# Performance work log

Measured on AMD Instinct MI355X. Metric: run time of the kernel, lower is better.

## Reference

```python
import jax, jax.numpy as jnp
import numpy as np

DIM = 512
HEADS = 8
HEAD_DIM = DIM // HEADS
SCALE = HEAD_DIM ** -0.5
CPB_HIDDEN = 512
N_CLASSES = 2
LN_EPS = 1e-5


def _layernorm(x, g, b):
    m = jnp.mean(x, axis=-1, keepdims=True)
    v = jnp.var(x, axis=-1, keepdims=True)
    return (x - m) / jnp.sqrt(v + LN_EPS) * g + b


def _coord_attention(x, coords, cpb_w1, cpb_b1, cpb_w2, cpb_b2, qkv_w, qkv_b, proj_w, proj_b):
    B, N, C = x.shape
    qkv = (x @ qkv_w + qkv_b).reshape(B, N, 3, HEADS, HEAD_DIM)
    q, k, v = jnp.moveaxis(qkv, 2, 0)  # each (B, N, H, hd)
    attn = jnp.einsum('bnhd,bmhd->bhnm', q * SCALE, k)  # (B, H, N, N)
    rel = coords[:, :, None, :] - coords[:, None, :, :]  # (B, N, N, 2)
    rel = rel / (jnp.linalg.norm(rel, axis=-1, keepdims=True) + 1e-6)
    bias = jax.nn.relu(rel @ cpb_w1 + cpb_b1) @ cpb_w2 + cpb_b2  # (B, N, N, H)
    attn = jax.nn.softmax(attn + jnp.transpose(bias, (0, 3, 1, 2)), axis=-1)
    out = jnp.einsum('bhnm,bmhd->bnhd', attn, v).reshape(B, N, C)
    return out @ proj_w + proj_b


def setup_inputs() -> dict:
    key = jax.random.key(0)
    ks = iter(jax.random.split(key, 32))
    d = {}
    d['h'] = jax.random.normal(next(ks), (1, 400, 1024), dtype=jnp.float32)
    d['coords'] = jax.random.uniform(next(ks), (1, 400, 2), dtype=jnp.float32) * 1000.0
    def lin(kw, kb, fan_in, fan_out):
        w = jax.random.normal(kw, (fan_in, fan_out), dtype=jnp.float32) / np.sqrt(fan_in)
        b = jax.random.normal(kb, (fan_out,), dtype=jnp.float32) * 0.01
        return w, b
    d['fc1_w'], d['fc1_b'] = lin(next(ks), next(ks), 1024, DIM)
    d['cls_token'] = jax.random.normal(next(ks), (1, 1, DIM), dtype=jnp.float32)
    for p in ('l1', 'l2'):
        d[p + '_norm_g'] = jnp.ones((DIM,), jnp.float32)
        d[p + '_norm_b'] = jnp.zeros((DIM,), jnp.float32)
        d[p + '_cpb_w1'], d[p + '_cpb_b1'] = lin(next(ks), next(ks), 2, CPB_HIDDEN)
        d[p + '_cpb_w2'], d[p + '_cpb_b2'] = lin(next(ks), next(ks), CPB_HIDDEN, HEADS)
        d[p + '_qkv_w'], d[p + '_qkv_b'] = lin(next(ks), next(ks), DIM, 3 * DIM)
        d[p + '_proj_w'], d[p + '_proj_b'] = lin(next(ks), next(ks), DIM, DIM)
    d['norm_g'] = jnp.ones((DIM,), jnp.float32)
    d['norm_b'] = jnp.zeros((DIM,), jnp.float32)
    d['fc2_w'], d['fc2_b'] = lin(next(ks), next(ks), DIM, N_CLASSES)
    return d


def reference(h, coords, fc1_w, fc1_b, cls_token,
              l1_norm_g, l1_norm_b, l1_cpb_w1, l1_cpb_b1, l1_cpb_w2, l1_cpb_b2,
              l1_qkv_w, l1_qkv_b, l1_proj_w, l1_proj_b,
              l2_norm_g, l2_norm_b, l2_cpb_w1, l2_cpb_b1, l2_cpb_w2, l2_cpb_b2,
              l2_qkv_w, l2_qkv_b, l2_proj_w, l2_proj_b,
              norm_g, norm_b, fc2_w, fc2_b):
    B, Np, _ = h.shape
    h = jax.nn.relu(h @ fc1_w + fc1_b)  # (B, N, 512)
    side = int(np.ceil(np.sqrt(Np)))
    add = side * side - Np  # pad bag to a perfect square (wrap-around copy)
    h = jnp.concatenate([h, h[:, :add, :]], axis=1)
    coords = jnp.concatenate([coords, coords[:, :add, :]], axis=1)
    cls = jnp.broadcast_to(cls_token, (B, 1, DIM))
    h = jnp.concatenate([cls, h], axis=1)
    coords = jnp.concatenate([jnp.zeros((B, 1, 2), h.dtype), coords], axis=1)
    h = h + _coord_attention(_layernorm(h, l1_norm_g, l1_norm_b), coords,
                             l1_cpb_w1, l1_cpb_b1, l1_cpb_w2, l1_cpb_b2,
                             l1_qkv_w, l1_qkv_b, l1_proj_w, l1_proj_b)
    h = h + _coord_attention(_layernorm(h, l2_norm_g, l2_norm_b), coords,
                             l2_cpb_w1, l2_cpb_b1, l2_cpb_w2, l2_cpb_b2,
                             l2_qkv_w, l2_qkv_b, l2_proj_w, l2_proj_b)
    h = _layernorm(h, norm_g, norm_b)[:, 0]  # CLS token
    return h @ fc2_w + fc2_b  # (B, n_classes)
```

## Files before the change

### kernel.cpp

```cpp
#include <hip/hip_runtime.h>
#include <math.h>

#define NP 401
#define DIM 512
#define LN_EPS 1e-5f
#define ATT_SCALE 0.125f
#define CPB_M 4096
#define TSTRIDE (CPB_M + 64)
#define PQS (401L * 1536)
#define PKS (401L * 1024)
#define PVS (401L * 512)

template<bool TB, typename LA, typename LB>
__device__ __forceinline__ void gemm64(
    int kBeg, int kEnd, int tid,
    float (*as)[68], float (*bs)[68], float (&acc)[4][4],
    LA&& loadA, LB&& loadB)
{
    float aR[4], bR[4];
    loadA(kBeg, aR);
    loadB(kBeg, bR);
    for (int k0 = kBeg; k0 < kEnd; k0 += 16) {
        const int arow = tid >> 2, aq = tid & 3;
        as[aq * 4 + 0][arow] = aR[0];
        as[aq * 4 + 1][arow] = aR[1];
        as[aq * 4 + 2][arow] = aR[2];
        as[aq * 4 + 3][arow] = aR[3];
        if (!TB) {
            *(float4*)&bs[tid >> 4][(tid & 15) * 4] =
                make_float4(bR[0], bR[1], bR[2], bR[3]);
        } else {
            bs[aq * 4 + 0][arow] = bR[0];
            bs[aq * 4 + 1][arow] = bR[1];
            bs[aq * 4 + 2][arow] = bR[2];
            bs[aq * 4 + 3][arow] = bR[3];
        }
        __syncthreads();
        float nA[4] = {0.f,0.f,0.f,0.f}, nB[4] = {0.f,0.f,0.f,0.f};
        if (k0 + 16 < kEnd) { loadA(k0 + 16, nA); loadB(k0 + 16, nB); }
        const int tx = tid & 15, ty = tid >> 4;
        #pragma unroll
        for (int kk = 0; kk < 16; ++kk) {
            float4 a4 = *(const float4*)&as[kk][ty * 4];
            float4 b4 = *(const float4*)&bs[kk][tx * 4];
            float av[4] = {a4.x, a4.y, a4.z, a4.w};
            float bv[4] = {b4.x, b4.y, b4.z, b4.w};
            #pragma unroll
            for (int r = 0; r < 4; ++r)
                #pragma unroll
                for (int c = 0; c < 4; ++c)
                    acc[r][c] = fmaf(av[r], bv[c], acc[r][c]);
        }
        __syncthreads();
        #pragma unroll
        for (int j = 0; j < 4; ++j) { aR[j] = nA[j]; bR[j] = nB[j]; }
    }
}

__global__ __launch_bounds__(256) void gemm_split_kernel(
    const float* __restrict__ A, int lda,
    const float* __restrict__ B, int ldb,
    float* __restrict__ P, int ldc, long slice,
    int M, int N, int K, int skN)
{
    __shared__ float as[16][68], bs[16][68];
    const int tid = threadIdx.x;
    const int m0 = blockIdx.x * 64, n0 = blockIdx.y * 64;
    const int sk = blockIdx.z;
    const int KS = ((K + skN * 16 - 1) / (skN * 16)) * 16;
    const int kBeg = sk * KS;
    const int kEnd = (kBeg + KS < K) ? kBeg + KS : K;
    float acc[4][4] = {};

    auto loadA = [&](int k0, float r[4]) {
        r[0] = r[1] = r[2] = r[3] = 0.f;
        int gm = m0 + (tid >> 2);
        if (gm >= M) return;
        int gk = k0 + (tid & 3) * 4;
        const float* p = A + (long)gm * lda + gk;
        if (gk + 3 < kEnd) {
            float4 v = *(const float4*)p;
            r[0] = v.x; r[1] = v.y; r[2] = v.z; r[3] = v.w;
        } else {
            #pragma unroll
            for (int j = 0; j < 4; ++j) if (gk + j < kEnd) r[j] = p[j];
        }
    };
    auto loadB = [&](int k0, float r[4]) {
        r[0] = r[1] = r[2] = r[3] = 0.f;
        int gk = k0 + (tid >> 4);
        if (gk >= kEnd) return;
        int gn = n0 + (tid & 15) * 4;
        const float* p = B + (long)gk * ldb + gn;
        float4 v = *(const float4*)p;
        r[0] = v.x; r[1] = v.y; r[2] = v.z; r[3] = v.w;
    };
    if (kBeg < kEnd)
        gemm64<false>(kBeg, kEnd, tid, as, bs, acc, loadA, loadB);

    float* C = P + (long)sk * slice;
    const int tx = tid & 15, ty = tid >> 4;
    #pragma unroll
    for (int r = 0; r < 4; ++r) {
        int m = m0 + ty * 4 + r;
        if (m >= M) continue;
        *(float4*)&C[(long)m * ldc + n0 + tx * 4] =
            make_float4(acc[r][0], acc[r][1], acc[r][2], acc[r][3]);
    }
}

__global__ __launch_bounds__(256) void reduce_kernel(
    const float* __restrict__ P, long slice, int skN,
    const float* __restrict__ bias, float* __restrict__ out,
    int total, int N)
{
    int idx = (blockIdx.x * 256 + threadIdx.x) * 4;
    if (idx >= total) return;
    float4 s = *(const float4*)(P + idx);
    for (int k = 1; k < skN; ++k) {
        float4 p = *(const float4*)(P + (long)k * slice + idx);
        s.x += p.x; s.y += p.y; s.z += p.z; s.w += p.w;
    }
    if (bias) {
        const float4 b = *(const float4*)(bias + (idx % N));
        s.x += b.x; s.y += b.y; s.z += b.z; s.w += b.w;
    }
    *(float4*)(out + idx) = s;
}

__global__ __launch_bounds__(256) void flash_kernel(
    const float* __restrict__ qkv,
    const int* __restrict__ pm, const float* __restrict__ pf,
    const float* __restrict__ T,
    float* __restrict__ PO,
    float* __restrict__ Pml)
{
    __shared__ float as[16][68], bs[16][68];
    __shared__ float pT[64][68];
    __shared__ float vs[64][68];
    const int tid = threadIdx.x;
    const int m0 = blockIdx.x * 64, nb = blockIdx.y, h = blockIdx.z;
    const int n0 = nb * 64;
    float acc[4][4] = {};

    float vreg[4][4];
    {
        int key = n0 + (tid >> 2);
        int d0 = (tid & 3) * 16;
        if (key <= 400) {
            const float* p = qkv + (long)key * 1536 + 1024 + h * 64 + d0;
            #pragma unroll
            for (int i = 0; i < 4; ++i) {
                float4 v = *(const float4*)(p + i * 4);
                vreg[i][0] = v.x; vreg[i][1] = v.y;
                vreg[i][2] = v.z; vreg[i][3] = v.w;
            }
        } else {
            #pragma unroll
            for (int i = 0; i < 4; ++i)
                vreg[i][0] = vreg[i][1] = vreg[i][2] = vreg[i][3] = 0.f;
        }
    }

    auto loadQ = [&](int k0, float r[4]) {
        int gm = m0 + (tid >> 2);
        if (gm > 400) { r[0]=r[1]=r[2]=r[3]=0.f; return; }
        int gk = k0 + (tid & 3) * 4;
        float4 v = *(const float4*)(qkv + (long)gm * 1536 + h * 64 + gk);
        r[0]=v.x; r[1]=v.y; r[2]=v.z; r[3]=v.w;
    };
    auto loadK = [&](int k0, float r[4]) {
        int gn = n0 + (tid >> 2);
        if (gn > 400) { r[0]=r[1]=r[2]=r[3]=0.f; return; }
        int gk = k0 + (tid & 3) * 4;
        float4 v = *(const float4*)(qkv + (long)gn * 1536 + 512 + h * 64 + gk);
        r[0]=v.x; r[1]=v.y; r[2]=v.z; r[3]=v.w;
    };
    gemm64<true>(0, 64, tid, as, bs, acc, loadQ, loadK);

    {
        int key = tid >> 2, d0 = (tid & 3) * 16;
        #pragma unroll
        for (int i = 0; i < 4; ++i)
            *(float4*)&vs[key][d0 + i * 4] =
                make_float4(vreg[i][0], vreg[i][1], vreg[i][2], vreg[i][3]);
    }

    const int tx = tid & 15, ty = tid >> 4;
    const float* Tt = T + (long)h * TSTRIDE;
    float p[4][4];
    #pragma unroll
    for (int r = 0; r < 4; ++r) {
        int i = m0 + ty * 4 + r;
        float sv[4];
        #pragma unroll
        for (int c = 0; c < 4; ++c) {
            int j = n0 + tx * 4 + c;
            if (i <= 400 && j <= 400) {
                int id = i * 416 + j;
                int mm = pm[id];
                float fr = pf[id];
                float t0 = Tt[mm], t1 = Tt[mm + 1];
                sv[c] = fmaf(acc[r][c], ATT_SCALE, fmaf(fr, t1 - t0, t0));
            } else {
                sv[c] = -INFINITY;
            }
        }
        float cmax = fmaxf(fmaxf(sv[0], sv[1]), fmaxf(sv[2], sv[3]));
        cmax = fmaxf(cmax, __shfl_xor(cmax, 1));
        cmax = fmaxf(cmax, __shfl_xor(cmax, 2));
        cmax = fmaxf(cmax, __shfl_xor(cmax, 4));
        cmax = fmaxf(cmax, __shfl_xor(cmax, 8));
        const bool rowok = (i <= 400);
        #pragma unroll
        for (int c = 0; c < 4; ++c)
            p[r][c] = rowok ? __expf(sv[c] - cmax) : 0.f;
        float cs = p[r][0] + p[r][1] + p[r][2] + p[r][3];
        cs += __shfl_xor(cs, 1);
        cs += __shfl_xor(cs, 2);
        cs += __shfl_xor(cs, 4);
        cs += __shfl_xor(cs, 8);
        if (tx == 0 && rowok) {
            long o = ((long)(h * 401 + i) * 7 + nb) * 2;
            Pml[o] = cmax;
            Pml[o + 1] = cs;
        }
    }
    #pragma unroll
    for (int c = 0; c < 4; ++c)
        *(float4*)&pT[tx * 4 + c][ty * 4] =
            make_float4(p[0][c], p[1][c], p[2][c], p[3][c]);
    __syncthreads();

    float o[4][4] = {};
    #pragma unroll 16
    for (int kk = 0; kk < 64; ++kk) {
        float4 a4 = *(const float4*)&pT[kk][ty * 4];
        float4 b4 = *(const float4*)&vs[kk][tx * 4];
        float av[4] = {a4.x, a4.y, a4.z, a4.w};
        float bv[4] = {b4.x, b4.y, b4.z, b4.w};
        #pragma unroll
        for (int r = 0; r < 4; ++r)
            #pragma unroll
            for (int c = 0; c < 4; ++c)
                o[r][c] = fmaf(av[r], bv[c], o[r][c]);
    }

    float* C = PO + (long)nb * PVS;
    #pragma unroll
    for (int r = 0; r < 4; ++r) {
        int m = m0 + ty * 4 + r;
        if (m > 400) continue;
        *(float4*)&C[(long)m * 512 + h * 64 + tx * 4] =
            make_float4(o[r][0], o[r][1], o[r][2], o[r][3]);
    }
}

__global__ __launch_bounds__(256) void proj_kernel(
    const float* __restrict__ PO, const float* __restrict__ Pml,
    const float* __restrict__ projw, float* __restrict__ Pp)
{
    __shared__ float as[16][68], bs[16][68];
    __shared__ float wls[64][8];
    const int tid = threadIdx.x;
    const int m0 = blockIdx.x * 64, n0 = blockIdx.y * 64, sk = blockIdx.z;
    const int kBeg = sk * 64, kEnd = kBeg + 64;
    float acc[4][4] = {};

    if (tid < 64) {
        int row = m0 + tid;
        if (row <= 400) {
            const float* q = Pml + ((long)(sk * 401 + row) * 7) * 2;
            float M = -INFINITY;
            #pragma unroll
            for (int c = 0; c < 7; ++c) M = fmaxf(M, q[c * 2]);
            float D = 0.f;
            #pragma unroll
            for (int c = 0; c < 7; ++c) D += q[c * 2 + 1] * __expf(q[c * 2] - M);
            float iD = 1.f / D;
            #pragma unroll
            for (int c = 0; c < 7; ++c) wls[tid][c] = __expf(q[c * 2] - M) * iD;
        } else {
            #pragma unroll
            for (int c = 0; c < 7; ++c) wls[tid][c] = 0.f;
        }
    }
    __syncthreads();

    auto loadA = [&](int k0, float r4[4]) {
        r4[0] = r4[1] = r4[2] = r4[3] = 0.f;
        int lm = tid >> 2, gm = m0 + lm;
        if (gm > 400) return;
        int gk = k0 + (tid & 3) * 4;
        #pragma unroll
        for (int s = 0; s < 7; ++s) {
            float4 v = *(const float4*)(PO + (long)s * PVS + (long)gm * 512 + gk);
            float w = wls[lm][s];
            r4[0] = fmaf(w, v.x, r4[0]);
            r4[1] = fmaf(w, v.y, r4[1]);
            r4[2] = fmaf(w, v.z, r4[2]);
            r4[3] = fmaf(w, v.w, r4[3]);
        }
    };
    auto loadB = [&](int k0, float r[4]) {
        int gk = k0 + (tid >> 4);
        int gn = n0 + (tid & 15) * 4;
        float4 v = *(const float4*)(projw + (long)gk * 512 + gn);
        r[0]=v.x; r[1]=v.y; r[2]=v.z; r[3]=v.w;
    };
    gemm64<false>(kBeg, kEnd, tid, as, bs, acc, loadA, loadB);

    float* C = Pp + (long)sk * PVS;
    const int tx = tid & 15, ty = tid >> 4;
    #pragma unroll
    for (int r = 0; r < 4; ++r) {
        int m = m0 + ty * 4 + r;
        if (m > 400) continue;
        *(float4*)&C[(long)m * 512 + n0 + tx * 4] =
            make_float4(acc[r][0], acc[r][1], acc[r][2], acc[r][3]);
    }
}

__global__ __launch_bounds__(256) void rowfuse_kernel(
    const float* __restrict__ P, long slice, int skN, int rowOff,
    const float* __restrict__ bias, int doRelu,
    const float* __restrict__ resid, const float* __restrict__ cls,
    float* __restrict__ h0,
    const float* __restrict__ g, const float* __restrict__ b,
    float* __restrict__ xln)
{
    const int r = blockIdx.x, t = threadIdx.x;
    float v0, v1;
    if (cls && r == 0) {
        v0 = cls[t]; v1 = cls[t + 256];
    } else {
        const float* p = P + (long)(r - rowOff) * DIM;
        v0 = bias[t]; v1 = bias[t + 256];
        for (int k = 0; k < skN; ++k) {
            v0 += p[(long)k * slice + t];
            v1 += p[(long)k * slice + t + 256];
        }
        if (resid) {
            v0 += resid[(long)r * DIM + t];
            v1 += resid[(long)r * DIM + t + 256];
        }
        if (doRelu) { v0 = fmaxf(v0, 0.f); v1 = fmaxf(v1, 0.f); }
    }
    h0[(long)r * DIM + t] = v0;
    h0[(long)r * DIM + t + 256] = v1;

    float s = v0 + v1, sq = v0 * v0 + v1 * v1;
    #pragma unroll
    for (int off = 32; off > 0; off >>= 1) {
        s += __shfl_down(s, off);
        sq += __shfl_down(sq, off);
    }
    __shared__ float ps[4], pq[4];
    int w = t >> 6, lane = t & 63;
    if (lane == 0) { ps[w] = s; pq[w] = sq; }
    __syncthreads();
    float Sm = ps[0] + ps[1] + ps[2] + ps[3];
    float Q = pq[0] + pq[1] + pq[2] + pq[3];
    float mean = Sm * (1.f / DIM);
    float var = Q * (1.f / DIM) - mean * mean;
    float inv = rsqrtf(var + LN_EPS);
    xln[(long)r * DIM + t]       = (v0 - mean) * inv * g[t] + b[t];
    xln[(long)r * DIM + t + 256] = (v1 - mean) * inv * g[t + 256] + b[t + 256];
}

__global__ __launch_bounds__(256) void cls_decode_kernel(
    const float* __restrict__ xln, const float* __restrict__ qkvw,
    const float* __restrict__ Pkv, const float* __restrict__ qkvb,
    const int* __restrict__ pm, const float* __restrict__ pf,
    const float* __restrict__ T,
    float* __restrict__ cms, float* __restrict__ cpv,
    unsigned* __restrict__ cnt)
{
    const int h = blockIdx.x, c = blockIdx.y, tid = threadIdx.x;
    const int kBeg = c * 64;
    __shared__ float q0[64], scraw[64], p[64], red[4][64], rr[2];

    if (h == 0 && c == 0 && tid == 0) *cnt = 0u;

    {
        int d = tid & 63, w4 = tid >> 6;
        const float* col = qkvw + h * 64 + d;
        float acc = 0.f;
        for (int k = w4 * 128; k < w4 * 128 + 128; ++k)
            acc = fmaf(xln[k], col[(long)k * 1536], acc);
        red[w4][d] = acc;
    }
    __syncthreads();
    if (tid < 64)
        q0[tid] = red[0][tid] + red[1][tid] + red[2][tid] + red[3][tid]
                  + qkvb[h * 64 + tid];
    __syncthreads();

    {
        int k = tid >> 2, q = tid & 3;
        int j = kBeg + k;
        float dot = 0.f;
        if (j < NP) {
            long base = (long)j * 1024 + h * 64 + q * 16;
            #pragma unroll
            for (int d = 0; d < 16; d += 4) {
                float4 x0 = *(const float4*)(Pkv + base + d);
                float4 x1 = *(const float4*)(Pkv + PKS + base + d);
                float4 x2 = *(const float4*)(Pkv + 2 * PKS + base + d);
                float4 x3 = *(const float4*)(Pkv + 3 * PKS + base + d);
                float4 bb = *(const float4*)(qkvb + 512 + h * 64 + q * 16 + d);
                float4 qq = *(const float4*)(q0 + q * 16 + d);
                dot = fmaf(qq.x, x0.x + x1.x + x2.x + x3.x + bb.x, dot);
                dot = fmaf(qq.y, x0.y + x1.y + x2.y + x3.y + bb.y, dot);
                dot = fmaf(qq.z, x0.z + x1.z + x2.z + x3.z + bb.z, dot);
                dot = fmaf(qq.w, x0.w + x1.w + x2.w + x3.w + bb.w, dot);
            }
        }
        dot += __shfl_down(dot, 2);
        dot += __shfl_down(dot, 1);
        if (q == 0) scraw[k] = dot;
    }
    __syncthreads();

    if (tid < 64) {
        int j = kBeg + tid;
        float s;
        if (j < NP) {
            int mm = pm[j];
            float fr = pf[j];
            const float* Tt = T + (long)h * TSTRIDE;
            float t0 = Tt[mm], t1 = Tt[mm + 1];
            s = fmaf(scraw[tid], ATT_SCALE, fmaf(fr, t1 - t0, t0));
        } else {
            s = -INFINITY;
        }
        float m = s;
        #pragma unroll
        for (int off = 32; off > 0; off >>= 1)
            m = fmaxf(m, __shfl_xor(m, off));
        float e = (j < NP) ? __expf(s - m) : 0.f;
        float sum = e;
        #pragma unroll
        for (int off = 32; off > 0; off >>= 1)
            sum += __shfl_xor(sum, off);
        p[tid] = e;
        if (tid == 0) { rr[0] = m; rr[1] = sum; }
    }
    __syncthreads();

    {
        int w = tid >> 6, d = tid & 63;
        float vb = qkvb[1024 + h * 64 + d];
        float acc = 0.f;
        for (int k = w; k < 64; k += 4) {
            int j = kBeg + k;
            if (j >= NP) break;
            long o = (long)j * 1024 + 512 + h * 64 + d;
            float v = Pkv[o] + Pkv[PKS + o] + Pkv[2 * PKS + o]
                      + Pkv[3 * PKS + o] + vb;
            acc = fmaf(p[k], v, acc);
        }
        red[w][d] = acc;
    }
    __syncthreads();
    if (tid < 64) {
        cpv[((long)h * 7 + c) * 64 + tid] =
            red[0][tid] + red[1][tid] + red[2][tid] + red[3][tid];
        if (tid == 0) {
            cms[(h * 7 + c) * 2 + 0] = rr[0];
            cms[(h * 7 + c) * 2 + 1] = rr[1];
        }
    }
}

__global__ __launch_bounds__(256) void cls_proj_kernel(
    const float* __restrict__ cms, const float* __restrict__ cpv,
    const float* __restrict__ projw, const float* __restrict__ projb,
    float* __restrict__ proj0,
    const float* __restrict__ h0,
    const float* __restrict__ g, const float* __restrict__ b,
    const float* __restrict__ fc2w, const float* __restrict__ fc2b,
    float* __restrict__ out, unsigned* __restrict__ cnt)
{
    __shared__ float av[512], red[4][64];
    __shared__ int isLast;
    const int bk = blockIdx.x, tid = threadIdx.x;
    for (int d = tid; d < 512; d += 256) {
        int h = d >> 6, dd = d & 63;
        float M = -INFINITY;
        #pragma unroll
        for (int c = 0; c < 7; ++c)
            M = fmaxf(M, cms[(h * 7 + c) * 2]);
        float Sx = 0.f, acc = 0.f;
        #pragma unroll
        for (int c = 0; c < 7; ++c) {
            float e = __expf(cms[(h * 7 + c) * 2] - M);
            Sx += cms[(h * 7 + c) * 2 + 1] * e;
            acc += cpv[((long)h * 7 + c) * 64 + dd] * e;
        }
        av[d] = acc / Sx;
    }
    __syncthreads();
    int gg = tid >> 6, n = bk * 64 + (tid & 63);
    float acc = 0.f;
    for (int k = gg * 128; k < gg * 128 + 128; ++k)
        acc = fmaf(av[k], projw[(long)k * 512 + n], acc);
    red[gg][tid & 63] = acc;
    __syncthreads();
    if (tid < 64)
        proj0[bk * 64 + tid] = red[0][tid] + red[1][tid] + red[2][tid]
                               + red[3][tid] + projb[bk * 64 + tid];

    __threadfence();
    if (tid == 0) isLast = (atomicAdd(cnt, 1u) == 7u);
    __syncthreads();
    if (!isLast) return;
    __threadfence();

    const int t = tid;
    float v0 = h0[t] + proj0[t];
    float v1 = h0[t + 256] + proj0[t + 256];
    float s = v0 + v1, sq = v0 * v0 + v1 * v1;
    #pragma unroll
    for (int off = 32; off > 0; off >>= 1) {
        s += __shfl_down(s, off);
        sq += __shfl_down(sq, off);
    }
    __shared__ float ps[4], pq[4], pc0[4], pc1[4];
    int w = t >> 6, lane = t & 63;
    if (lane == 0) { ps[w] = s; pq[w] = sq; }
    __syncthreads();
    float Sm = ps[0] + ps[1] + ps[2] + ps[3];
    float Q = pq[0] + pq[1] + pq[2] + pq[3];
    float mean = Sm * (1.f / DIM);
    float var = Q * (1.f / DIM) - mean * mean;
    float inv = rsqrtf(var + LN_EPS);
    float n0 = (v0 - mean) * inv * g[t] + b[t];
    float n1 = (v1 - mean) * inv * g[t + 256] + b[t + 256];
    float c0 = n0 * fc2w[t * 2]     + n1 * fc2w[(t + 256) * 2];
    float c1 = n0 * fc2w[t * 2 + 1] + n1 * fc2w[(t + 256) * 2 + 1];
    #pragma unroll
    for (int off = 32; off > 0; off >>= 1) {
        c0 += __shfl_down(c0, off);
        c1 += __shfl_down(c1, off);
    }
    if (lane == 0) { pc0[w] = c0; pc1[w] = c1; }
    __syncthreads();
    if (t == 0) {
        out[0] = pc0[0] + pc0[1] + pc0[2] + pc0[3] + fc2b[0];
        out[1] = pc1[0] + pc1[1] + pc1[2] + pc1[3] + fc2b[1];
    }
}

__global__ __launch_bounds__(256) void mega_kernel(
    const float* __restrict__ hin, const float* __restrict__ fc1_w,
    const float* __restrict__ w1_0, const float* __restrict__ b1_0,
    const float* __restrict__ w2_0, const float* __restrict__ b2_0,
    const float* __restrict__ w1_1, const float* __restrict__ b1_1,
    const float* __restrict__ w2_1, const float* __restrict__ b2_1,
    const float* __restrict__ coords,
    float* __restrict__ Pp, float* __restrict__ T,
    int* __restrict__ pm, float* __restrict__ pf)
{
    __shared__ float smem[2176];
    float (*as)[68] = (float(*)[68])smem;
    float (*bs)[68] = (float(*)[68])(smem + 1088);
    float (*red)[64][8] = (float(*)[64][8])smem;
    const int bid = blockIdx.x, tid = threadIdx.x;

    if (bid < 896) {
        int sk = bid / 56, rem = bid % 56;
        int m0 = (rem % 7) * 64, n0 = (rem / 7) * 64;
        int kBeg = sk * 64, kEnd = kBeg + 64;
        float acc[4][4] = {};
        auto loadA = [&](int k0, float r[4]) {
            r[0]=r[1]=r[2]=r[3]=0.f;
            int gm = m0 + (tid >> 2);
            if (gm >= 400) return;
            int gk = k0 + (tid & 3) * 4;
            float4 v = *(const float4*)(hin + (long)gm * 1024 + gk);
            r[0]=v.x; r[1]=v.y; r[2]=v.z; r[3]=v.w;
        };
        auto loadB = [&](int k0, float r[4]) {
            int gk = k0 + (tid >> 4);
            int gn = n0 + (tid & 15) * 4;
            float4 v = *(const float4*)(fc1_w + (long)gk * 512 + gn);
            r[0]=v.x; r[1]=v.y; r[2]=v.z; r[3]=v.w;
        };
        gemm64<false>(kBeg, kEnd, tid, as, bs, acc, loadA, loadB);
        float* C = Pp + (long)sk * PVS;
        const int tx = tid & 15, ty = tid >> 4;
        #pragma unroll
        for (int r = 0; r < 4; ++r) {
            int m = m0 + ty * 4 + r;
            if (m >= 400) continue;
            *(float4*)&C[(long)m * 512 + n0 + tx * 4] =
                make_float4(acc[r][0], acc[r][1], acc[r][2], acc[r][3]);
        }
    } else if (bid < 1026) {
        int tb = bid - 896;
        int z = tb / 65, ab = tb % 65;
        const float* w1 = z ? w1_1 : w1_0;
        const float* b1 = z ? b1_1 : b1_0;
        const float* w2 = z ? w2_1 : w2_0;
        const float* b2 = z ? b2_1 : b2_0;
        const int lane = tid & 63, wv = tid >> 6;
        float ca = 0.f, sa = 0.f;
        if (ab != 64) {
            float th = fmaf((float)(ab * 64 + lane),
                            (float)(2.0 * M_PI / CPB_M), -(float)M_PI);
            sincosf(th, &sa, &ca);
        } else if (lane == 0) {
            sincosf((float)M_PI, &sa, &ca);
        }
        float a8[8] = {};
        const int kbeg = wv * 128;
        #pragma unroll 4
        for (int k = kbeg; k < kbeg + 128; ++k) {
            float hk = fmaxf(fmaf(ca, w1[k],
                                  fmaf(sa, w1[512 + k], b1[k])), 0.f);
            #pragma unroll
            for (int h2 = 0; h2 < 8; ++h2)
                a8[h2] = fmaf(hk, w2[k * 8 + h2], a8[h2]);
        }
        #pragma unroll
        for (int h2 = 0; h2 < 8; ++h2) red[wv][lane][h2] = a8[h2];
        __syncthreads();
        if (tid < 64) {
            int aidx = ab * 64 + tid;
            if (aidx <= CPB_M + 1) {
                #pragma unroll
                for (int h2 = 0; h2 < 8; ++h2)
                    T[(long)(z * 8 + h2) * TSTRIDE + aidx] =
                        red[0][tid][h2] + red[1][tid][h2] +
                        red[2][tid][h2] + red[3][tid][h2] + b2[h2];
            }
        }
    } else {
        int p = (bid - 1026) * 256 + tid;
        if (p < NP * NP) {
            int i = p / NP, j = p - i * NP;
            float xi = (i == 0) ? 0.f : coords[(i - 1) * 2];
            float yi = (i == 0) ? 0.f : coords[(i - 1) * 2 + 1];
            float xj = (j == 0) ? 0.f : coords[(j - 1) * 2];
            float yj = (j == 0) ? 0.f : coords[(j - 1) * 2 + 1];
            float rx = xi - xj, ry = yi - yj;
            int mm; float fr;
            if (rx == 0.f && ry == 0.f) {
                mm = CPB_M + 1; fr = 0.f;
            } else {
                float x = (atan2f(ry, rx) + 3.14159265358979f)
                          * (float)(CPB_M / (2.0 * M_PI));
                int mi = (int)x;
                fr = x - (float)mi;
                mm = (mi >= CPB_M) ? mi - CPB_M : mi;
            }
            pm[i * 416 + j] = mm;
            pf[i * 416 + j] = fr;
        }
    }
}

extern "C" void kernel_launch(void* const* d_in, const int* in_sizes, int n_in,
                              void* d_out, int out_size, void* d_ws, size_t ws_size,
                              hipStream_t stream)
{
    const float* coords = (const float*)d_in[1];
    float* ws = (float*)d_ws;
    float* h0   = ws;                    ws += 401L * 512;
    float* xln  = ws;                    ws += 401L * 512;
    float* PO   = ws;                    ws += 7L * PVS;
    float* T    = ws;                    ws += 16L * TSTRIDE;
    int*   pm   = (int*)ws;              ws += 401L * 416;
    float* pf   = ws;                    ws += 401L * 416;
    float* Pq   = ws;                    ws += 4L * PQS;
    float* qkv  = ws;                    ws += 401L * 1536;
    float* Pp   = ws;                    ws += 16L * PVS;
    float* proj0 = ws;                   ws += 512;
    float* cms  = ws;                    ws += 8L * 7 * 2;
    float* cpv  = ws;                    ws += 8L * 7 * 64;
    float* Pml  = ws;                    ws += 8L * 401 * 7 * 2;
    unsigned* cnt = (unsigned*)ws;       ws += 16;

    mega_kernel<<<1655, 256, 0, stream>>>(
        (const float*)d_in[0], (const float*)d_in[2],
        (const float*)d_in[7],  (const float*)d_in[8],
        (const float*)d_in[9],  (const float*)d_in[10],
        (const float*)d_in[17], (const float*)d_in[18],
        (const float*)d_in[19], (const float*)d_in[20],
        coords, Pp, T, pm, pf);

    rowfuse_kernel<<<401, 256, 0, stream>>>(
        Pp, PVS, 16, 1, (const float*)d_in[3], 1, nullptr,
        (const float*)d_in[4], h0,
        (const float*)d_in[5], (const float*)d_in[6], xln);

    gemm_split_kernel<<<dim3(7, 24, 4), 256, 0, stream>>>(
        xln, 512, (const float*)d_in[11], 1536, Pq, 1536, PQS,
        401, 1536, 512, 4);
    reduce_kernel<<<602, 256, 0, stream>>>(
        Pq, PQS, 4, (const float*)d_in[12], qkv, 401 * 1536, 1536);
    flash_kernel<<<dim3(7, 7, 8), 256, 0, stream>>>(
        qkv, pm, pf, T, PO, Pml);
    proj_kernel<<<dim3(7, 8, 8), 256, 0, stream>>>(
        PO, Pml, (const float*)d_in[13], Pp);
    rowfuse_kernel<<<401, 256, 0, stream>>>(
        Pp, PVS, 8, 0, (const float*)d_in[14], 0, h0, nullptr, h0,
        (const float*)d_in[15], (const float*)d_in[16], xln);

    gemm_split_kernel<<<dim3(7, 16, 4), 256, 0, stream>>>(
        xln, 512, (const float*)d_in[21] + 512, 1536, Pq, 1024, PKS,
        401, 1024, 512, 4);
    cls_decode_kernel<<<dim3(8, 7), 256, 0, stream>>>(
        xln, (const float*)d_in[21], Pq, (const float*)d_in[22],
        pm, pf, T + 8L * TSTRIDE, cms, cpv, cnt);
    cls_proj_kernel<<<8, 256, 0, stream>>>(
        cms, cpv, (const float*)d_in[23], (const float*)d_in[24], proj0,
        h0, (const float*)d_in[25], (const float*)d_in[26],
        (const float*)d_in[27], (const float*)d_in[28], (float*)d_out, cnt);
}
```

Measured before the change: 241.3 us.

## Drop split-K partial sums for QKV/KV GEMMs and fuse bias into epilogue

Replaces the split-K GEMM plus separate reduce kernel with a single full-K GEMM that adds the bias directly, so one launch and the partial-sum round trip through global memory go away. The layer-2 KV projection now writes final values, which simplifies cls_decode loads. The fc1 split-K inside mega_kernel drops from 16 to 4 slices, shrinking partial buffers and rowfuse reduction work. The cost is fewer blocks (168/112 instead of 4x that), which lowers parallelism on a large GPU and leaves each block with a longer serial K loop.

```diff
diff --git a/kernel.cpp b/kernel.cpp
--- a/kernel.cpp
+++ b/kernel.cpp
@@ -7,8 +7,6 @@
 #define ATT_SCALE 0.125f
 #define CPB_M 4096
 #define TSTRIDE (CPB_M + 64)
-#define PQS (401L * 1536)
-#define PKS (401L * 1024)
 #define PVS (401L * 512)
 
 template<bool TB, typename LA, typename LB>
@@ -57,75 +55,42 @@
     }
 }
 
-__global__ __launch_bounds__(256) void gemm_split_kernel(
-    const float* __restrict__ A, int lda,
+__global__ __launch_bounds__(256) void gemm_bias_kernel(
+    const float* __restrict__ A,
     const float* __restrict__ B, int ldb,
-    float* __restrict__ P, int ldc, long slice,
-    int M, int N, int K, int skN)
+    const float* __restrict__ bias,
+    float* __restrict__ C, int ldc)
 {
     __shared__ float as[16][68], bs[16][68];
     const int tid = threadIdx.x;
     const int m0 = blockIdx.x * 64, n0 = blockIdx.y * 64;
-    const int sk = blockIdx.z;
-    const int KS = ((K + skN * 16 - 1) / (skN * 16)) * 16;
-    const int kBeg = sk * KS;
-    const int kEnd = (kBeg + KS < K) ? kBeg + KS : K;
     float acc[4][4] = {};
 
     auto loadA = [&](int k0, float r[4]) {
-        r[0] = r[1] = r[2] = r[3] = 0.f;
         int gm = m0 + (tid >> 2);
-        if (gm >= M) return;
+        if (gm > 400) { r[0]=r[1]=r[2]=r[3]=0.f; return; }
         int gk = k0 + (tid & 3) * 4;
-        const float* p = A + (long)gm * lda + gk;
-        if (gk + 3 < kEnd) {
-            float4 v = *(const float4*)p;
-            r[0] = v.x; r[1] = v.y; r[2] = v.z; r[3] = v.w;
-        } else {
-            #pragma unroll
-            for (int j = 0; j < 4; ++j) if (gk + j < kEnd) r[j] = p[j];
-        }
+        float4 v = *(const float4*)(A + (long)gm * 512 + gk);
+        r[0]=v.x; r[1]=v.y; r[2]=v.z; r[3]=v.w;
     };
     auto loadB = [&](int k0, float r[4]) {
-        r[0] = r[1] = r[2] = r[3] = 0.f;
         int gk = k0 + (tid >> 4);
-        if (gk >= kEnd) return;
         int gn = n0 + (tid & 15) * 4;
-        const float* p = B + (long)gk * ldb + gn;
-        float4 v = *(const float4*)p;
-        r[0] = v.x; r[1] = v.y; r[2] = v.z; r[3] = v.w;
+        float4 v = *(const float4*)(B + (long)gk * ldb + gn);
+        r[0]=v.x; r[1]=v.y; r[2]=v.z; r[3]=v.w;
     };
-    if (kBeg < kEnd)
-        gemm64<false>(kBeg, kEnd, tid, as, bs, acc, loadA, loadB);
-
-    float* C = P + (long)sk * slice;
+    gemm64<false>(0, 512, tid, as, bs, acc, loadA, loadB);
+
     const int tx = tid & 15, ty = tid >> 4;
+    const float4 bv = *(const float4*)(bias + n0 + tx * 4);
     #pragma unroll
     for (int r = 0; r < 4; ++r) {
         int m = m0 + ty * 4 + r;
-        if (m >= M) continue;
+        if (m > 400) continue;
         *(float4*)&C[(long)m * ldc + n0 + tx * 4] =
-            make_float4(acc[r][0], acc[r][1], acc[r][2], acc[r][3]);
-    }
-}
-
-__global__ __launch_bounds__(256) void reduce_kernel(
-    const float* __restrict__ P, long slice, int skN,
-    const float* __restrict__ bias, float* __restrict__ out,
-    int total, int N)
-{
-    int idx = (blockIdx.x * 256 + threadIdx.x) * 4;
-    if (idx >= total) return;
-    float4 s = *(const float4*)(P + idx);
-    for (int k = 1; k < skN; ++k) {
-        float4 p = *(const float4*)(P + (long)k * slice + idx);
-        s.x += p.x; s.y += p.y; s.z += p.z; s.w += p.w;
-    }
-    if (bias) {
-        const float4 b = *(const float4*)(bias + (idx % N));
-        s.x += b.x; s.y += b.y; s.z += b.z; s.w += b.w;
-    }
-    *(float4*)(out + idx) = s;
+            make_float4(acc[r][0] + bv.x, acc[r][1] + bv.y,
+                        acc[r][2] + bv.z, acc[r][3] + bv.w);
+    }
 }
 
 __global__ __launch_bounds__(256) void flash_kernel(
@@ -370,7 +335,7 @@
 
 __global__ __launch_bounds__(256) void cls_decode_kernel(
     const float* __restrict__ xln, const float* __restrict__ qkvw,
-    const float* __restrict__ Pkv, const float* __restrict__ qkvb,
+    const float* __restrict__ kv, const float* __restrict__ qkvb,
     const int* __restrict__ pm, const float* __restrict__ pf,
     const float* __restrict__ T,
     float* __restrict__ cms, float* __restrict__ cpv,
@@ -404,16 +369,12 @@
             long base = (long)j * 1024 + h * 64 + q * 16;
             #pragma unroll
             for (int d = 0; d < 16; d += 4) {
-                float4 x0 = *(const float4*)(Pkv + base + d);
-                float4 x1 = *(const float4*)(Pkv + PKS + base + d);
-                float4 x2 = *(const float4*)(Pkv + 2 * PKS + base + d);
-                float4 x3 = *(const float4*)(Pkv + 3 * PKS + base + d);
-                float4 bb = *(const float4*)(qkvb + 512 + h * 64 + q * 16 + d);
+                float4 x0 = *(const float4*)(kv + base + d);
                 float4 qq = *(const float4*)(q0 + q * 16 + d);
-                dot = fmaf(qq.x, x0.x + x1.x + x2.x + x3.x + bb.x, dot);
-                dot = fmaf(qq.y, x0.y + x1.y + x2.y + x3.y + bb.y, dot);
-                dot = fmaf(qq.z, x0.z + x1.z + x2.z + x3.z + bb.z, dot);
-                dot = fmaf(qq.w, x0.w + x1.w + x2.w + x3.w + bb.w, dot);
+                dot = fmaf(qq.x, x0.x, dot);
+                dot = fmaf(qq.y, x0.y, dot);
+                dot = fmaf(qq.z, x0.z, dot);
+                dot = fmaf(qq.w, x0.w, dot);
             }
         }
         dot += __shfl_down(dot, 2);
@@ -450,15 +411,12 @@
 
     {
         int w = tid >> 6, d = tid & 63;
-        float vb = qkvb[1024 + h * 64 + d];
         float acc = 0.f;
         for (int k = w; k < 64; k += 4) {
             int j = kBeg + k;
             if (j >= NP) break;
             long o = (long)j * 1024 + 512 + h * 64 + d;
-            float v = Pkv[o] + Pkv[PKS + o] + Pkv[2 * PKS + o]
-                      + Pkv[3 * PKS + o] + vb;
-            acc = fmaf(p[k], v, acc);
+            acc = fmaf(p[k], kv[o], acc);
         }
         red[w][d] = acc;
     }
@@ -568,10 +526,10 @@
     float (*red)[64][8] = (float(*)[64][8])smem;
     const int bid = blockIdx.x, tid = threadIdx.x;
 
-    if (bid < 896) {
+    if (bid < 224) {
         int sk = bid / 56, rem = bid % 56;
         int m0 = (rem % 7) * 64, n0 = (rem / 7) * 64;
-        int kBeg = sk * 64, kEnd = kBeg + 64;
+        int kBeg = sk * 256, kEnd = kBeg + 256;
         float acc[4][4] = {};
         auto loadA = [&](int k0, float r[4]) {
             r[0]=r[1]=r[2]=r[3]=0.f;
@@ -597,8 +555,8 @@
             *(float4*)&C[(long)m * 512 + n0 + tx * 4] =
                 make_float4(acc[r][0], acc[r][1], acc[r][2], acc[r][3]);
         }
-    } else if (bid < 1026) {
-        int tb = bid - 896;
+    } else if (bid < 354) {
+        int tb = bid - 224;
         int z = tb / 65, ab = tb % 65;
         const float* w1 = z ? w1_1 : w1_0;
         const float* b1 = z ? b1_1 : b1_0;
@@ -637,7 +595,7 @@
             }
         }
     } else {
-        int p = (bid - 1026) * 256 + tid;
+        int p = (bid - 354) * 256 + tid;
         if (p < NP * NP) {
             int i = p / NP, j = p - i * NP;
             float xi = (i == 0) ? 0.f : coords[(i - 1) * 2];
@@ -673,16 +631,16 @@
     float* T    = ws;                    ws += 16L * TSTRIDE;
     int*   pm   = (int*)ws;              ws += 401L * 416;
     float* pf   = ws;                    ws += 401L * 416;
-    float* Pq   = ws;                    ws += 4L * PQS;
+    float* kv   = ws;                    ws += 401L * 1024;
     float* qkv  = ws;                    ws += 401L * 1536;
-    float* Pp   = ws;                    ws += 16L * PVS;
+    float* Pp   = ws;                    ws += 8L * PVS;
     float* proj0 = ws;                   ws += 512;
     float* cms  = ws;                    ws += 8L * 7 * 2;
     float* cpv  = ws;                    ws += 8L * 7 * 64;
     float* Pml  = ws;                    ws += 8L * 401 * 7 * 2;
     unsigned* cnt = (unsigned*)ws;       ws += 16;
 
-    mega_kernel<<<1655, 256, 0, stream>>>(
+    mega_kernel<<<983, 256, 0, stream>>>(
         (const float*)d_in[0], (const float*)d_in[2],
         (const float*)d_in[7],  (const float*)d_in[8],
         (const float*)d_in[9],  (const float*)d_in[10],
@@ -691,15 +649,13 @@
         coords, Pp, T, pm, pf);
 
     rowfuse_kernel<<<401, 256, 0, stream>>>(
-        Pp, PVS, 16, 1, (const float*)d_in[3], 1, nullptr,
+        Pp, PVS, 4, 1, (const float*)d_in[3], 1, nullptr,
         (const float*)d_in[4], h0,
         (const float*)d_in[5], (const float*)d_in[6], xln);
 
-    gemm_split_kernel<<<dim3(7, 24, 4), 256, 0, stream>>>(
-        xln, 512, (const float*)d_in[11], 1536, Pq, 1536, PQS,
-        401, 1536, 512, 4);
-    reduce_kernel<<<602, 256, 0, stream>>>(
-        Pq, PQS, 4, (const float*)d_in[12], qkv, 401 * 1536, 1536);
+    gemm_bias_kernel<<<dim3(7, 24), 256, 0, stream>>>(
+        xln, (const float*)d_in[11], 1536, (const float*)d_in[12],
+        qkv, 1536);
     flash_kernel<<<dim3(7, 7, 8), 256, 0, stream>>>(
         qkv, pm, pf, T, PO, Pml);
     proj_kernel<<<dim3(7, 8, 8), 256, 0, stream>>>(
@@ -708,11 +664,11 @@
         Pp, PVS, 8, 0, (const float*)d_in[14], 0, h0, nullptr, h0,
         (const float*)d_in[15], (const float*)d_in[16], xln);
 
-    gemm_split_kernel<<<dim3(7, 16, 4), 256, 0, stream>>>(
-        xln, 512, (const float*)d_in[21] + 512, 1536, Pq, 1024, PKS,
-        401, 1024, 512, 4);
+    gemm_bias_kernel<<<dim3(7, 16), 256, 0, stream>>>(
+        xln, (const float*)d_in[21] + 512, 1536, (const float*)d_in[22] + 512,
+        kv, 1024);
     cls_decode_kernel<<<dim3(8, 7), 256, 0, stream>>>(
-        xln, (const float*)d_in[21], Pq, (const float*)d_in[22],
+        xln, (const float*)d_in[21], kv, (const float*)d_in[22],
         pm, pf, T + 8L * TSTRIDE, cms, cpv, cnt);
     cls_proj_kernel<<<8, 256, 0, stream>>>(
         cms, cpv, (const float*)d_in[23], (const float*)d_in[24], proj0,
```

New measurement: 242.7 us. No clear change (+0.6%).

## Fuse QKV split-K reduction into flash kernel loads and halve fc1 split-K

Applied to the files above, without the earlier changes.

Removes the separate reduce_kernel launch by having the flash kernel sum the four split-K partial slices plus the QKV bias directly when loading Q, K and V tiles. Separately, the fc1 GEMM in the mega kernel uses 8 split-K slices of 128 instead of 16 slices of 64, which halves partial-sum traffic and the rowfuse reduction work. In exchange, each Q/K tile is re-reduced by every block that loads it, which multiplies global reads in flash, and the fc1 GEMM has fewer blocks available for parallelism.

```diff
diff --git a/kernel.cpp b/kernel.cpp
--- a/kernel.cpp
+++ b/kernel.cpp
@@ -109,27 +109,9 @@
     }
 }
 
-__global__ __launch_bounds__(256) void reduce_kernel(
-    const float* __restrict__ P, long slice, int skN,
-    const float* __restrict__ bias, float* __restrict__ out,
-    int total, int N)
-{
-    int idx = (blockIdx.x * 256 + threadIdx.x) * 4;
-    if (idx >= total) return;
-    float4 s = *(const float4*)(P + idx);
-    for (int k = 1; k < skN; ++k) {
-        float4 p = *(const float4*)(P + (long)k * slice + idx);
-        s.x += p.x; s.y += p.y; s.z += p.z; s.w += p.w;
-    }
-    if (bias) {
-        const float4 b = *(const float4*)(bias + (idx % N));
-        s.x += b.x; s.y += b.y; s.z += b.z; s.w += b.w;
-    }
-    *(float4*)(out + idx) = s;
-}
-
 __global__ __launch_bounds__(256) void flash_kernel(
-    const float* __restrict__ qkv,
+    const float* __restrict__ Pq,
+    const float* __restrict__ qkvb,
     const int* __restrict__ pm, const float* __restrict__ pf,
     const float* __restrict__ T,
     float* __restrict__ PO,
@@ -148,12 +130,18 @@
         int key = n0 + (tid >> 2);
         int d0 = (tid & 3) * 16;
         if (key <= 400) {
-            const float* p = qkv + (long)key * 1536 + 1024 + h * 64 + d0;
+            long base = (long)key * 1536 + 1024 + h * 64 + d0;
             #pragma unroll
             for (int i = 0; i < 4; ++i) {
-                float4 v = *(const float4*)(p + i * 4);
-                vreg[i][0] = v.x; vreg[i][1] = v.y;
-                vreg[i][2] = v.z; vreg[i][3] = v.w;
+                float4 v0 = *(const float4*)(Pq + base + i * 4);
+                float4 v1 = *(const float4*)(Pq + PQS + base + i * 4);
+                float4 v2 = *(const float4*)(Pq + 2 * PQS + base + i * 4);
+                float4 v3 = *(const float4*)(Pq + 3 * PQS + base + i * 4);
+                float4 bb = *(const float4*)(qkvb + 1024 + h * 64 + d0 + i * 4);
+                vreg[i][0] = v0.x + v1.x + v2.x + v3.x + bb.x;
+                vreg[i][1] = v0.y + v1.y + v2.y + v3.y + bb.y;
+                vreg[i][2] = v0.z + v1.z + v2.z + v3.z + bb.z;
+                vreg[i][3] = v0.w + v1.w + v2.w + v3.w + bb.w;
             }
         } else {
             #pragma unroll
@@ -166,15 +154,31 @@
         int gm = m0 + (tid >> 2);
         if (gm > 400) { r[0]=r[1]=r[2]=r[3]=0.f; return; }
         int gk = k0 + (tid & 3) * 4;
-        float4 v = *(const float4*)(qkv + (long)gm * 1536 + h * 64 + gk);
-        r[0]=v.x; r[1]=v.y; r[2]=v.z; r[3]=v.w;
+        long base = (long)gm * 1536 + h * 64 + gk;
+        float4 v0 = *(const float4*)(Pq + base);
+        float4 v1 = *(const float4*)(Pq + PQS + base);
+        float4 v2 = *(const float4*)(Pq + 2 * PQS + base);
+        float4 v3 = *(const float4*)(Pq + 3 * PQS + base);
+        float4 bb = *(const float4*)(qkvb + h * 64 + gk);
+        r[0] = v0.x + v1.x + v2.x + v3.x + bb.x;
+        r[1] = v0.y + v1.y + v2.y + v3.y + bb.y;
+        r[2] = v0.z + v1.z + v2.z + v3.z + bb.z;
+        r[3] = v0.w + v1.w + v2.w + v3.w + bb.w;
     };
     auto loadK = [&](int k0, float r[4]) {
         int gn = n0 + (tid >> 2);
         if (gn > 400) { r[0]=r[1]=r[2]=r[3]=0.f; return; }
         int gk = k0 + (tid & 3) * 4;
-        float4 v = *(const float4*)(qkv + (long)gn * 1536 + 512 + h * 64 + gk);
-        r[0]=v.x; r[1]=v.y; r[2]=v.z; r[3]=v.w;
+        long base = (long)gn * 1536 + 512 + h * 64 + gk;
+        float4 v0 = *(const float4*)(Pq + base);
+        float4 v1 = *(const float4*)(Pq + PQS + base);
+        float4 v2 = *(const float4*)(Pq + 2 * PQS + base);
+        float4 v3 = *(const float4*)(Pq + 3 * PQS + base);
+        float4 bb = *(const float4*)(qkvb + 512 + h * 64 + gk);
+        r[0] = v0.x + v1.x + v2.x + v3.x + bb.x;
+        r[1] = v0.y + v1.y + v2.y + v3.y + bb.y;
+        r[2] = v0.z + v1.z + v2.z + v3.z + bb.z;
+        r[3] = v0.w + v1.w + v2.w + v3.w + bb.w;
     };
     gemm64<true>(0, 64, tid, as, bs, acc, loadQ, loadK);
 
@@ -568,10 +572,10 @@
     float (*red)[64][8] = (float(*)[64][8])smem;
     const int bid = blockIdx.x, tid = threadIdx.x;
 
-    if (bid < 896) {
+    if (bid < 448) {
         int sk = bid / 56, rem = bid % 56;
         int m0 = (rem % 7) * 64, n0 = (rem / 7) * 64;
-        int kBeg = sk * 64, kEnd = kBeg + 64;
+        int kBeg = sk * 128, kEnd = kBeg + 128;
         float acc[4][4] = {};
         auto loadA = [&](int k0, float r[4]) {
             r[0]=r[1]=r[2]=r[3]=0.f;
@@ -597,8 +601,8 @@
             *(float4*)&C[(long)m * 512 + n0 + tx * 4] =
                 make_float4(acc[r][0], acc[r][1], acc[r][2], acc[r][3]);
         }
-    } else if (bid < 1026) {
-        int tb = bid - 896;
+    } else if (bid < 578) {
+        int tb = bid - 448;
         int z = tb / 65, ab = tb % 65;
         const float* w1 = z ? w1_1 : w1_0;
         const float* b1 = z ? b1_1 : b1_0;
@@ -637,7 +641,7 @@
             }
         }
     } else {
-        int p = (bid - 1026) * 256 + tid;
+        int p = (bid - 578) * 256 + tid;
         if (p < NP * NP) {
             int i = p / NP, j = p - i * NP;
             float xi = (i == 0) ? 0.f : coords[(i - 1) * 2];
@@ -674,15 +678,14 @@
     int*   pm   = (int*)ws;              ws += 401L * 416;
     float* pf   = ws;                    ws += 401L * 416;
     float* Pq   = ws;                    ws += 4L * PQS;
-    float* qkv  = ws;                    ws += 401L * 1536;
-    float* Pp   = ws;                    ws += 16L * PVS;
+    float* Pp   = ws;                    ws += 8L * PVS;
     float* proj0 = ws;                   ws += 512;
     float* cms  = ws;                    ws += 8L * 7 * 2;
     float* cpv  = ws;                    ws += 8L * 7 * 64;
     float* Pml  = ws;                    ws += 8L * 401 * 7 * 2;
     unsigned* cnt = (unsigned*)ws;       ws += 16;
 
-    mega_kernel<<<1655, 256, 0, stream>>>(
+    mega_kernel<<<1207, 256, 0, stream>>>(
         (const float*)d_in[0], (const float*)d_in[2],
         (const float*)d_in[7],  (const float*)d_in[8],
         (const float*)d_in[9],  (const float*)d_in[10],
@@ -691,17 +694,15 @@
         coords, Pp, T, pm, pf);
 
     rowfuse_kernel<<<401, 256, 0, stream>>>(
-        Pp, PVS, 16, 1, (const float*)d_in[3], 1, nullptr,
+        Pp, PVS, 8, 1, (const float*)d_in[3], 1, nullptr,
         (const float*)d_in[4], h0,
         (const float*)d_in[5], (const float*)d_in[6], xln);
 
     gemm_split_kernel<<<dim3(7, 24, 4), 256, 0, stream>>>(
         xln, 512, (const float*)d_in[11], 1536, Pq, 1536, PQS,
         401, 1536, 512, 4);
-    reduce_kernel<<<602, 256, 0, stream>>>(
-        Pq, PQS, 4, (const float*)d_in[12], qkv, 401 * 1536, 1536);
     flash_kernel<<<dim3(7, 7, 8), 256, 0, stream>>>(
-        qkv, pm, pf, T, PO, Pml);
+        Pq, (const float*)d_in[12], pm, pf, T, PO, Pml);
     proj_kernel<<<dim3(7, 8, 8), 256, 0, stream>>>(
         PO, Pml, (const float*)d_in[13], Pp);
     rowfuse_kernel<<<401, 256, 0, stream>>>(
```

Result: no change. 237.3 us (-1.6%).
